# Kernel optimization log

Measured on AMD Instinct MI355X. Metric: run time of the kernel, lower is better.

The kernel has to match this reference:

```python
import math
import jax, jax.numpy as jnp
import numpy as np

TAU = 2.0
THR = 1.0
ALPHA = 10.0

T, B, IN_DIM, OUT_DIM = 64, 128, 2048, 2048


def setup_inputs() -> dict:
    key = jax.random.key(0)
    k1, k2, k3 = jax.random.split(key, 3)
    x_seq = jax.random.normal(k1, (T, B, IN_DIM), dtype=jnp.float32)
    # scale like nn.Linear default init so membrane potentials are O(1)
    W = jax.random.normal(k2, (OUT_DIM, IN_DIM), dtype=jnp.float32) / math.sqrt(IN_DIM)
    b = jax.random.normal(k3, (OUT_DIM,), dtype=jnp.float32) * 0.01
    return {"x_seq": x_seq, "W": W, "b": b}


def spike(x):
    # forward: hard threshold (surrogate gradient only matters in bwd)
    return (x > 0).astype(x.dtype)


def reference(x_seq, W, b):
    decay = math.exp(-1.0 / TAU)
    # hoist the linear layer out of the recurrence: one big GEMM
    cur_seq = jnp.einsum("tbi,oi->tbo", x_seq, W) + b  # (T, B, OUT_DIM)
    mem0 = jnp.zeros((x_seq.shape[1], W.shape[0]), dtype=x_seq.dtype)

    def step(mem, cur):
        mem = mem * decay + cur
        spk = spike(mem - THR)
        mem = mem - spk * THR
        return mem, spk

    _, spk_seq = jax.lax.scan(step, mem0, cur_seq)
    return spk_seq  # (T, B, OUT_DIM)
```

## Files before the change

### kernel.cpp

```cpp
#include <hip/hip_runtime.h>
#include <hip/hip_bf16.h>
#include <math.h>


typedef unsigned short u16;
typedef __attribute__((ext_vector_type(8))) short bf16x8;
typedef __attribute__((ext_vector_type(4))) float f32x4;

constexpr int T_STEPS = 64;
constexpr int BATCH   = 128;
constexpr int K_DIM   = 2048;
constexpr int N_DIM   = 2048;
constexpr int M_DIM   = T_STEPS * BATCH;
constexpr int NCHAIN  = BATCH * N_DIM;

constexpr float DECAY_F32 = (float)0.6065306597126334;
constexpr float BAND      = 2e-4f;

__global__ __launch_bounds__(512, 2)
void gemm_lif(const float* __restrict__ X, const float* __restrict__ W,
              const float* __restrict__ bias, float* __restrict__ out,
              unsigned int* __restrict__ counters,
              unsigned int* __restrict__ worklist) {
    extern __shared__ __align__(16) u16 smem[];
    u16* const sAh = smem;
    u16* const sAl = smem + 2 * 8192;
    u16* const sBh = smem + 4 * 8192;
    u16* const sBl = smem + 4 * 8192 + 2 * 4096;

    const int tid  = threadIdx.x;
    const int orig = blockIdx.x + gridDim.x * blockIdx.y;
    const int wg   = (orig & 7) * 64 + (orig >> 3);
    const int b0i  = (wg >> 4) * 4;
    const int n0   = (wg & 15) * 128;
    const int lane = tid & 63;
    const int wave = tid >> 6;
    const int wm   = wave >> 1;
    const int wn   = wave & 1;

    const int re   = (tid >> 6) * 16 + (tid & 15);
    const int ks_e = ((tid >> 4) & 3) * 8;
    const size_t a0f = (size_t)((re >> 2) * 128 + b0i + (re & 3)) * K_DIM + ks_e;
    const size_t a1f = (size_t)(((re >> 2) + 32) * 128 + b0i + (re & 3)) * K_DIM + ks_e;
    const size_t b0f = (size_t)(n0 + re) * K_DIM + ks_e;
    const int wA0 = tid * 8;
    const int wA1 = 4096 + tid * 8;
    const int wB0 = tid * 8;

    f32x4 acc[4][4];
#pragma unroll
    for (int i = 0; i < 4; i++)
#pragma unroll
        for (int j = 0; j < 4; j++) acc[i][j] = (f32x4){0.f, 0.f, 0.f, 0.f};

    float4 g0[6], g1[6];

#define GLOAD(SET, kc) do {                                                  \
        const size_t k_ = (size_t)(kc) * 32;                                 \
        g##SET[0] = *(const float4*)(X + a0f + k_);                          \
        g##SET[1] = *(const float4*)(X + a0f + k_ + 4);                      \
        g##SET[2] = *(const float4*)(X + a1f + k_);                          \
        g##SET[3] = *(const float4*)(X + a1f + k_ + 4);                      \
        g##SET[4] = *(const float4*)(W + b0f + k_);                          \
        g##SET[5] = *(const float4*)(W + b0f + k_ + 4);                      \
    } while (0)

#define DEK8(v0, v1, HI, LO) do {                                            \
        const float f_[8] = {v0.x, v0.y, v0.z, v0.w, v1.x, v1.y, v1.z, v1.w};\
        unsigned int hp_[4], lp_[4];                                         \
        _Pragma("unroll")                                                    \
        for (int q_ = 0; q_ < 8; q_ += 2) {                                  \
            u16 hh_[2], ll_[2];                                              \
            _Pragma("unroll")                                                \
            for (int e_ = 0; e_ < 2; e_++) {                                 \
                __hip_bfloat16 hb_ = __float2bfloat16(f_[q_ + e_]);          \
                const float hf_ = __bfloat162float(hb_);                     \
                __hip_bfloat16 lb_ = __float2bfloat16(f_[q_ + e_] - hf_);    \
                hh_[e_] = *(u16*)&hb_;                                       \
                ll_[e_] = *(u16*)&lb_;                                       \
            }                                                                \
            hp_[q_ >> 1] = (unsigned int)hh_[0] | ((unsigned int)hh_[1] << 16); \
            lp_[q_ >> 1] = (unsigned int)ll_[0] | ((unsigned int)ll_[1] << 16); \
        }                                                                    \
        HI = make_uint4(hp_[0], hp_[1], hp_[2], hp_[3]);                     \
        LO = make_uint4(lp_[0], lp_[1], lp_[2], lp_[3]);                     \
    } while (0)

#define CONVWRITE(s, SET) do {                                               \
        uint4 hA0_, lA0_, hA1_, lA1_, hB_, lB_;                              \
        DEK8(g##SET[0], g##SET[1], hA0_, lA0_);                              \
        DEK8(g##SET[2], g##SET[3], hA1_, lA1_);                              \
        DEK8(g##SET[4], g##SET[5], hB_, lB_);                                \
        *(uint4*)&sAh[(s) * 8192 + wA0] = hA0_;                              \
        *(uint4*)&sAl[(s) * 8192 + wA0] = lA0_;                              \
        *(uint4*)&sAh[(s) * 8192 + wA1] = hA1_;                              \
        *(uint4*)&sAl[(s) * 8192 + wA1] = lA1_;                              \
        *(uint4*)&sBh[(s) * 4096 + wB0] = hB_;                               \
        *(uint4*)&sBl[(s) * 4096 + wB0] = lB_;                               \
    } while (0)

#define COMPUTE(rs) do {                                                     \
        bf16x8 fah[4], fal[4], fbh[4], fbl[4];                               \
        _Pragma("unroll")                                                    \
        for (int ti = 0; ti < 4; ti++) {                                     \
            const int ta = wm * 4 + ti;                                      \
            fah[ti] = *(const bf16x8*)&sAh[(rs) * 8192 + (ta * 64 + lane) * 8]; \
            fal[ti] = *(const bf16x8*)&sAl[(rs) * 8192 + (ta * 64 + lane) * 8]; \
        }                                                                    \
        _Pragma("unroll")                                                    \
        for (int tj = 0; tj < 4; tj++) {                                     \
            const int tb = wn * 4 + tj;                                      \
            fbh[tj] = *(const bf16x8*)&sBh[(rs) * 4096 + (tb * 64 + lane) * 8]; \
            fbl[tj] = *(const bf16x8*)&sBl[(rs) * 4096 + (tb * 64 + lane) * 8]; \
        }                                                                    \
        __builtin_amdgcn_s_setprio(1);                                       \
        _Pragma("unroll")                                                    \
        for (int ti = 0; ti < 4; ti++)                                       \
        _Pragma("unroll")                                                    \
        for (int tj = 0; tj < 4; tj++) {                                     \
            acc[ti][tj] = __builtin_amdgcn_mfma_f32_16x16x32_bf16(           \
                fah[ti], fbh[tj], acc[ti][tj], 0, 0, 0);                     \
            acc[ti][tj] = __builtin_amdgcn_mfma_f32_16x16x32_bf16(           \
                fah[ti], fbl[tj], acc[ti][tj], 0, 0, 0);                     \
            acc[ti][tj] = __builtin_amdgcn_mfma_f32_16x16x32_bf16(           \
                fal[ti], fbh[tj], acc[ti][tj], 0, 0, 0);                     \
        }                                                                    \
        __builtin_amdgcn_s_setprio(0);                                       \
    } while (0)

#define BAR do {                                                             \
        __builtin_amdgcn_sched_barrier(0);                                   \
        __builtin_amdgcn_s_barrier();                                        \
        __builtin_amdgcn_sched_barrier(0);                                   \
    } while (0)
#define VMW(n) do {                                                          \
        asm volatile("s_waitcnt vmcnt(" #n ")" ::: "memory");                \
        __builtin_amdgcn_sched_barrier(0);                                   \
    } while (0)
#define LGKM0 do {                                                           \
        asm volatile("s_waitcnt lgkmcnt(0)" ::: "memory");                   \
        __builtin_amdgcn_sched_barrier(0);                                   \
    } while (0)

    GLOAD(0, 0);
    VMW(0);
    CONVWRITE(0, 0);
    GLOAD(1, 1);
    LGKM0;

    for (int kc = 0; kc < 60; kc += 2) {
        BAR;
        GLOAD(0, kc + 2);
        VMW(6);
        CONVWRITE(1, 1);
        LGKM0;
        COMPUTE(0);
        BAR;
        GLOAD(1, kc + 3);
        VMW(6);
        CONVWRITE(0, 0);
        LGKM0;
        COMPUTE(1);
    }
    BAR;
    GLOAD(0, 62);
    VMW(6);
    CONVWRITE(1, 1);
    LGKM0;
    COMPUTE(0);
    BAR;
    GLOAD(1, 63);
    VMW(6);
    CONVWRITE(0, 0);
    LGKM0;
    COMPUTE(1);
    BAR;
    VMW(0);
    CONVWRITE(1, 1);
    LGKM0;
    COMPUTE(0);
    BAR;
    COMPUTE(1);

#undef LGKM0
#undef VMW
#undef BAR
#undef COMPUTE
#undef CONVWRITE
#undef DEK8
#undef GLOAD

    __syncthreads();
    float* const curL = (float*)smem;

#pragma unroll
    for (int tj = 0; tj < 4; tj++) {
        const int col = wn * 64 + tj * 16 + (lane & 15);
        const float bv = bias[n0 + col];
#pragma unroll
        for (int ti = 0; ti < 4; ti++) {
            const int rb = wm * 64 + ti * 16 + (lane >> 4) * 4;
#pragma unroll
            for (int r = 0; r < 4; r++)
                curL[(rb + r) * 129 + col] = acc[ti][tj][r] + bv;
        }
    }
    __syncthreads();

    {
        const int bl  = tid >> 7;
        const int col = tid & 127;
        const int b   = b0i + bl;
        const int o   = n0 + col;
        float mem = 0.0f;
        bool flag = false;
#pragma unroll
        for (int t = 0; t < T_STEPS; t++) {
            const float cv = curL[(t * 4 + bl) * 129 + col];
            mem = __fadd_rn(__fmul_rn(mem, DECAY_F32), cv);
            const float d = __fsub_rn(mem, 1.0f);
            const bool spk = d > 0.0f;
            if (fabsf(d) < BAND) flag = true;
            out[(size_t)t * NCHAIN + (size_t)b * N_DIM + o] = spk ? 1.0f : 0.0f;
            if (spk) mem = __fsub_rn(mem, 1.0f);
        }
        if (flag) {
            const unsigned int p = atomicAdd(&counters[b], 1u);
            worklist[b * 2048 + p] = (unsigned int)o;
        }
    }
}

#define RG 16
#define RJ 4
#define BKR 64

__global__ __launch_bounds__(256)
void lif_repair2(const float* __restrict__ X, const float* __restrict__ W,
                 const float* __restrict__ bias,
                 const unsigned int* __restrict__ counters,
                 const unsigned int* __restrict__ worklist,
                 float* __restrict__ out) {
    __shared__ float sX[BKR][T_STEPS + 1];
    __shared__ float sW[RG][BKR + 1];
    __shared__ float scur[T_STEPS][RG + 1];
    __shared__ float sspk[T_STEPS][RG + 1];
    __shared__ int   so[RG];

    const int b = blockIdx.x / RJ;
    const int j = blockIdx.x % RJ;
    const unsigned int n_b = counters[b];
    if (n_b == 0) return;
    const int ngroups = (int)(n_b + RG - 1) / RG;

    const int tid = threadIdx.x;
    const int t   = tid & 63;
    const int oi  = tid >> 6;

    const int ts  = tid >> 2;
    const int kq  = (tid & 3) * 16;
    const int wo  = tid >> 4;
    const int wkq = (tid & 15) * 4;

    for (int g = j; g < ngroups; g += RJ) {
        if (tid < RG) {
            const int slot = g * RG + tid;
            so[tid] = (slot < (int)n_b) ? (int)worklist[b * 2048 + slot] : -1;
        }
        __syncthreads();

        float Csum[4] = {0.f, 0.f, 0.f, 0.f};
        float P[4]    = {0.f, 0.f, 0.f, 0.f};

        float4 rx[4];
        float4 rw;
        {
            const float* srcx = &X[(size_t)(ts * BATCH + b) * K_DIM + kq];
#pragma unroll
            for (int q = 0; q < 4; q++) rx[q] = *(const float4*)(srcx + q * 4);
            const int o = so[wo];
            rw = (o >= 0) ? *(const float4*)&W[(size_t)o * K_DIM + wkq]
                          : make_float4(0.f, 0.f, 0.f, 0.f);
        }

        for (int c = 0; c < K_DIM / BKR; c++) {
            if (c > 0 && (c % 5) == 0) {
#pragma unroll
                for (int q = 0; q < 4; q++) {
                    Csum[q] = __fadd_rn(Csum[q], P[q]);
                    P[q] = 0.f;
                }
            }
            __syncthreads();
#pragma unroll
            for (int q = 0; q < 4; q++) {
                sX[kq + q * 4 + 0][ts] = rx[q].x;
                sX[kq + q * 4 + 1][ts] = rx[q].y;
                sX[kq + q * 4 + 2][ts] = rx[q].z;
                sX[kq + q * 4 + 3][ts] = rx[q].w;
            }
            sW[wo][wkq + 0] = rw.x; sW[wo][wkq + 1] = rw.y;
            sW[wo][wkq + 2] = rw.z; sW[wo][wkq + 3] = rw.w;
            if (c + 1 < K_DIM / BKR) {
                const int k1 = (c + 1) * BKR;
                const float* srcx = &X[(size_t)(ts * BATCH + b) * K_DIM + k1 + kq];
#pragma unroll
                for (int q = 0; q < 4; q++) rx[q] = *(const float4*)(srcx + q * 4);
                const int o = so[wo];
                rw = (o >= 0) ? *(const float4*)&W[(size_t)o * K_DIM + k1 + wkq]
                              : make_float4(0.f, 0.f, 0.f, 0.f);
            }
            __syncthreads();
#pragma unroll 8
            for (int k = 0; k < BKR; k++) {
                const float xv = sX[k][t];
#pragma unroll
                for (int q = 0; q < 4; q++)
                    P[q] = fmaf(xv, sW[oi * 4 + q][k], P[q]);
            }
        }
        __syncthreads();
#pragma unroll
        for (int q = 0; q < 4; q++) {
            Csum[q] = __fadd_rn(Csum[q], P[q]);
            const int o = so[oi * 4 + q];
            scur[t][oi * 4 + q] = (o >= 0) ? __fadd_rn(Csum[q], bias[o]) : 0.f;
        }
        __syncthreads();
        if (tid < RG && so[tid] >= 0) {
            float mem = 0.0f;
            for (int tt = 0; tt < T_STEPS; tt++) {
                mem = __fadd_rn(__fmul_rn(mem, DECAY_F32), scur[tt][tid]);
                const float d = __fsub_rn(mem, 1.0f);
                const bool spk = d > 0.0f;
                sspk[tt][tid] = spk ? 1.0f : 0.0f;
                if (spk) mem = __fsub_rn(mem, 1.0f);
            }
        }
        __syncthreads();
#pragma unroll
        for (int q = 0; q < 4; q++) {
            const int o = so[oi * 4 + q];
            if (o >= 0)
                out[(size_t)t * NCHAIN + (size_t)b * N_DIM + o] = sspk[t][oi * 4 + q];
        }
        __syncthreads();
    }
}

__global__ __launch_bounds__(256)
void lif_openblas_q320(const float* __restrict__ X, const float* __restrict__ W,
                       const float* __restrict__ bias, float* __restrict__ out) {
    __shared__ float As[16][T_STEPS + 4];
    __shared__ float Ws[16][64 + 4];
    __shared__ float curbuf[T_STEPS][64 + 1];
    const int tid = threadIdx.x;
    const int o0 = blockIdx.x * 64, b0 = blockIdx.y;
    const int tm = (tid & 15) * 4, tn = (tid >> 4) * 4;
    float Csum[4][4], Pacc[4][4];
#pragma unroll
    for (int i = 0; i < 4; i++)
#pragma unroll
        for (int j = 0; j < 4; j++) { Csum[i][j] = 0.f; Pacc[i][j] = 0.f; }
    for (int c = 0; c < K_DIM / 16; c++) {
        if (c > 0 && (c % 20) == 0) {
#pragma unroll
            for (int i = 0; i < 4; i++)
#pragma unroll
                for (int j = 0; j < 4; j++) {
                    Csum[i][j] = __fadd_rn(Csum[i][j], Pacc[i][j]);
                    Pacc[i][j] = 0.f;
                }
        }
        const int k0 = c * 16;
        {
            const int t = tid >> 2, kq = (tid & 3) * 4;
            const float4 av = *(const float4*)&X[(size_t)(t * BATCH + b0) * K_DIM + k0 + kq];
            As[kq + 0][t] = av.x; As[kq + 1][t] = av.y;
            As[kq + 2][t] = av.z; As[kq + 3][t] = av.w;
            const float4 wv = *(const float4*)&W[(size_t)(o0 + t) * K_DIM + k0 + kq];
            Ws[kq + 0][t] = wv.x; Ws[kq + 1][t] = wv.y;
            Ws[kq + 2][t] = wv.z; Ws[kq + 3][t] = wv.w;
        }
        __syncthreads();
#pragma unroll
        for (int k = 0; k < 16; k++) {
            float a[4], w[4];
#pragma unroll
            for (int i = 0; i < 4; i++) a[i] = As[k][tm + i];
#pragma unroll
            for (int j = 0; j < 4; j++) w[j] = Ws[k][tn + j];
#pragma unroll
            for (int i = 0; i < 4; i++)
#pragma unroll
                for (int j = 0; j < 4; j++) Pacc[i][j] = fmaf(a[i], w[j], Pacc[i][j]);
        }
        __syncthreads();
    }
#pragma unroll
    for (int i = 0; i < 4; i++)
#pragma unroll
        for (int j = 0; j < 4; j++)
            curbuf[tm + i][tn + j] =
                __fadd_rn(__fadd_rn(Csum[i][j], Pacc[i][j]), bias[o0 + tn + j]);
    __syncthreads();
    if (tid < 64) {
        float mem = 0.0f;
#pragma unroll
        for (int t = 0; t < T_STEPS; t++) {
            mem = __fadd_rn(__fmul_rn(mem, DECAY_F32), curbuf[t][tid]);
            const float d = __fsub_rn(mem, 1.0f);
            const bool spk = d > 0.0f;
            out[(size_t)t * NCHAIN + (size_t)b0 * N_DIM + o0 + tid] = spk ? 1.0f : 0.0f;
            if (spk) mem = __fsub_rn(mem, 1.0f);
        }
    }
}

extern "C" void kernel_launch(void* const* d_in, const int* in_sizes, int n_in,
                              void* d_out, int out_size, void* d_ws, size_t ws_size,
                              hipStream_t stream) {
    const float* x = nullptr; const float* W = nullptr; const float* bias = nullptr;
    for (int i = 0; i < n_in; i++) {
        if      (in_sizes[i] == M_DIM * K_DIM) x    = (const float*)d_in[i];
        else if (in_sizes[i] == N_DIM * K_DIM) W    = (const float*)d_in[i];
        else if (in_sizes[i] == N_DIM)         bias = (const float*)d_in[i];
    }
    if (!x)    x    = (const float*)d_in[0];
    if (!W)    W    = (const float*)d_in[1];
    if (!bias) bias = (const float*)d_in[2];
    float* out = (float*)d_out;

    const size_t off_cnt = 0;
    const size_t off_wl  = 512;
    const size_t need    = off_wl + (size_t)128 * 2048 * 4;

    if (ws_size < need) {
        dim3 grid(N_DIM / 64, BATCH);
        lif_openblas_q320<<<grid, 256, 0, stream>>>(x, W, bias, out);
        return;
    }

    char* ws = (char*)d_ws;
    unsigned int* counters = (unsigned int*)(ws + off_cnt);
    unsigned int* worklist = (unsigned int*)(ws + off_wl);

    hipMemsetAsync(counters, 0, 512, stream);

    dim3 ggrid(N_DIM / 128, M_DIM / 256);
    gemm_lif<<<ggrid, 512, 132096, stream>>>(x, W, bias, out, counters, worklist);
    lif_repair2<<<128 * RJ, 256, 0, stream>>>(x, W, bias, counters, worklist, out);
}
```

Before: 417.7 us.

## Pre-split W into bf16 hi/lo planes and stream B tiles via global_load_lds

A new prologue kernel converts W once per call into separate bf16 high and low planes in workspace, and also zeroes the counters, which replaces the memset. The GEMM kernel then loads B tiles directly into LDS with global_load_lds and a three-deep B buffer. A tiles are still converted in registers. This removes the repeated per-block fp32-to-bf16 split of W and the register staging for B, at the cost of an extra kernel launch and extra workspace traffic.

```diff
diff --git a/kernel.cpp b/kernel.cpp
--- a/kernel.cpp
+++ b/kernel.cpp
@@ -17,8 +17,40 @@
 constexpr float DECAY_F32 = (float)0.6065306597126334;
 constexpr float BAND      = 2e-4f;
 
+#define GLDS16(g, l) __builtin_amdgcn_global_load_lds(                       \
+    (const __attribute__((address_space(1))) void*)(g),                      \
+    (__attribute__((address_space(3))) void*)(l), 16, 0, 0)
+
+__global__ __launch_bounds__(256)
+void wsplit(const float* __restrict__ W, u16* __restrict__ Wh,
+            u16* __restrict__ Wl, unsigned int* __restrict__ counters) {
+    if (blockIdx.x == 0 && threadIdx.x < 128) counters[threadIdx.x] = 0u;
+    const int base = blockIdx.x * 256 + threadIdx.x;
+    const float4 v0 = *(const float4*)(W + (size_t)base * 8);
+    const float4 v1 = *(const float4*)(W + (size_t)base * 8 + 4);
+    const float f[8] = {v0.x, v0.y, v0.z, v0.w, v1.x, v1.y, v1.z, v1.w};
+    unsigned int hp[4], lp[4];
+#pragma unroll
+    for (int q = 0; q < 8; q += 2) {
+        u16 hh[2], ll[2];
+#pragma unroll
+        for (int e = 0; e < 2; e++) {
+            __hip_bfloat16 hb = __float2bfloat16(f[q + e]);
+            const float hf = __bfloat162float(hb);
+            __hip_bfloat16 lb = __float2bfloat16(f[q + e] - hf);
+            hh[e] = *(u16*)&hb;
+            ll[e] = *(u16*)&lb;
+        }
+        hp[q >> 1] = (unsigned int)hh[0] | ((unsigned int)hh[1] << 16);
+        lp[q >> 1] = (unsigned int)ll[0] | ((unsigned int)ll[1] << 16);
+    }
+    *(uint4*)(Wh + (size_t)base * 8) = make_uint4(hp[0], hp[1], hp[2], hp[3]);
+    *(uint4*)(Wl + (size_t)base * 8) = make_uint4(lp[0], lp[1], lp[2], lp[3]);
+}
+
 __global__ __launch_bounds__(512, 2)
-void gemm_lif(const float* __restrict__ X, const float* __restrict__ W,
+void gemm_lif(const float* __restrict__ X,
+              const u16* __restrict__ Bh, const u16* __restrict__ Bl,
               const float* __restrict__ bias, float* __restrict__ out,
               unsigned int* __restrict__ counters,
               unsigned int* __restrict__ worklist) {
@@ -26,7 +58,7 @@
     u16* const sAh = smem;
     u16* const sAl = smem + 2 * 8192;
     u16* const sBh = smem + 4 * 8192;
-    u16* const sBl = smem + 4 * 8192 + 2 * 4096;
+    u16* const sBl = smem + 4 * 8192 + 3 * 4096;
 
     const int tid  = threadIdx.x;
     const int orig = blockIdx.x + gridDim.x * blockIdx.y;
@@ -45,7 +77,7 @@
     const size_t b0f = (size_t)(n0 + re) * K_DIM + ks_e;
     const int wA0 = tid * 8;
     const int wA1 = 4096 + tid * 8;
-    const int wB0 = tid * 8;
+    const int lB0 = wave * 512;
 
     f32x4 acc[4][4];
 #pragma unroll
@@ -53,16 +85,20 @@
 #pragma unroll
         for (int j = 0; j < 4; j++) acc[i][j] = (f32x4){0.f, 0.f, 0.f, 0.f};
 
-    float4 g0[6], g1[6];
-
-#define GLOAD(SET, kc) do {                                                  \
+    float4 g0[4], g1[4];
+
+#define GLOADA(SET, kc) do {                                                 \
         const size_t k_ = (size_t)(kc) * 32;                                 \
         g##SET[0] = *(const float4*)(X + a0f + k_);                          \
         g##SET[1] = *(const float4*)(X + a0f + k_ + 4);                      \
         g##SET[2] = *(const float4*)(X + a1f + k_);                          \
         g##SET[3] = *(const float4*)(X + a1f + k_ + 4);                      \
-        g##SET[4] = *(const float4*)(W + b0f + k_);                          \
-        g##SET[5] = *(const float4*)(W + b0f + k_ + 4);                      \
+    } while (0)
+
+#define GLDSB(bs, kc) do {                                                   \
+        const size_t k_ = (size_t)(kc) * 32;                                 \
+        GLDS16(Bh + b0f + k_, sBh + (bs) * 4096 + lB0);                      \
+        GLDS16(Bl + b0f + k_, sBl + (bs) * 4096 + lB0);                      \
     } while (0)
 
 #define DEK8(v0, v1, HI, LO) do {                                            \
@@ -86,32 +122,29 @@
         LO = make_uint4(lp_[0], lp_[1], lp_[2], lp_[3]);                     \
     } while (0)
 
-#define CONVWRITE(s, SET) do {                                               \
-        uint4 hA0_, lA0_, hA1_, lA1_, hB_, lB_;                              \
+#define CONVWA(s, SET) do {                                                  \
+        uint4 hA0_, lA0_, hA1_, lA1_;                                        \
         DEK8(g##SET[0], g##SET[1], hA0_, lA0_);                              \
         DEK8(g##SET[2], g##SET[3], hA1_, lA1_);                              \
-        DEK8(g##SET[4], g##SET[5], hB_, lB_);                                \
         *(uint4*)&sAh[(s) * 8192 + wA0] = hA0_;                              \
         *(uint4*)&sAl[(s) * 8192 + wA0] = lA0_;                              \
         *(uint4*)&sAh[(s) * 8192 + wA1] = hA1_;                              \
         *(uint4*)&sAl[(s) * 8192 + wA1] = lA1_;                              \
-        *(uint4*)&sBh[(s) * 4096 + wB0] = hB_;                               \
-        *(uint4*)&sBl[(s) * 4096 + wB0] = lB_;                               \
-    } while (0)
-
-#define COMPUTE(rs) do {                                                     \
+    } while (0)
+
+#define COMPUTE(ra, rb) do {                                                 \
         bf16x8 fah[4], fal[4], fbh[4], fbl[4];                               \
         _Pragma("unroll")                                                    \
         for (int ti = 0; ti < 4; ti++) {                                     \
             const int ta = wm * 4 + ti;                                      \
-            fah[ti] = *(const bf16x8*)&sAh[(rs) * 8192 + (ta * 64 + lane) * 8]; \
-            fal[ti] = *(const bf16x8*)&sAl[(rs) * 8192 + (ta * 64 + lane) * 8]; \
+            fah[ti] = *(const bf16x8*)&sAh[(ra) * 8192 + (ta * 64 + lane) * 8]; \
+            fal[ti] = *(const bf16x8*)&sAl[(ra) * 8192 + (ta * 64 + lane) * 8]; \
         }                                                                    \
         _Pragma("unroll")                                                    \
         for (int tj = 0; tj < 4; tj++) {                                     \
             const int tb = wn * 4 + tj;                                      \
-            fbh[tj] = *(const bf16x8*)&sBh[(rs) * 4096 + (tb * 64 + lane) * 8]; \
-            fbl[tj] = *(const bf16x8*)&sBl[(rs) * 4096 + (tb * 64 + lane) * 8]; \
+            fbh[tj] = *(const bf16x8*)&sBh[(rb) * 4096 + (tb * 64 + lane) * 8]; \
+            fbl[tj] = *(const bf16x8*)&sBl[(rb) * 4096 + (tb * 64 + lane) * 8]; \
         }                                                                    \
         __builtin_amdgcn_s_setprio(1);                                       \
         _Pragma("unroll")                                                    \
@@ -142,53 +175,44 @@
         __builtin_amdgcn_sched_barrier(0);                                   \
     } while (0)
 
-    GLOAD(0, 0);
-    VMW(0);
-    CONVWRITE(0, 0);
-    GLOAD(1, 1);
+    GLOADA(0, 0);
+    GLDSB(0, 0);
+    GLOADA(1, 1);
+    GLDSB(1, 1);
+    VMW(6);
+    CONVWA(0, 0);
     LGKM0;
 
-    for (int kc = 0; kc < 60; kc += 2) {
-        BAR;
-        GLOAD(0, kc + 2);
-        VMW(6);
-        CONVWRITE(1, 1);
-        LGKM0;
-        COMPUTE(0);
-        BAR;
-        GLOAD(1, kc + 3);
-        VMW(6);
-        CONVWRITE(0, 0);
-        LGKM0;
-        COMPUTE(1);
-    }
-    BAR;
-    GLOAD(0, 62);
-    VMW(6);
-    CONVWRITE(1, 1);
-    LGKM0;
-    COMPUTE(0);
-    BAR;
-    GLOAD(1, 63);
-    VMW(6);
-    CONVWRITE(0, 0);
-    LGKM0;
-    COMPUTE(1);
-    BAR;
-    VMW(0);
-    CONVWRITE(1, 1);
-    LGKM0;
-    COMPUTE(0);
-    BAR;
-    COMPUTE(1);
+    for (int kcb = 0; kcb < 60; kcb += 6) {
+        BAR;  GLOADA(0, kcb + 2);  GLDSB(2, kcb + 2);  VMW(6);
+        CONVWA(1, 1);  LGKM0;  COMPUTE(0, 0);
+        BAR;  GLOADA(1, kcb + 3);  GLDSB(0, kcb + 3);  VMW(6);
+        CONVWA(0, 0);  LGKM0;  COMPUTE(1, 1);
+        BAR;  GLOADA(0, kcb + 4);  GLDSB(1, kcb + 4);  VMW(6);
+        CONVWA(1, 1);  LGKM0;  COMPUTE(0, 2);
+        BAR;  GLOADA(1, kcb + 5);  GLDSB(2, kcb + 5);  VMW(6);
+        CONVWA(0, 0);  LGKM0;  COMPUTE(1, 0);
+        BAR;  GLOADA(0, kcb + 6);  GLDSB(0, kcb + 6);  VMW(6);
+        CONVWA(1, 1);  LGKM0;  COMPUTE(0, 1);
+        BAR;  GLOADA(1, kcb + 7);  GLDSB(1, kcb + 7);  VMW(6);
+        CONVWA(0, 0);  LGKM0;  COMPUTE(1, 2);
+    }
+    BAR;  GLOADA(0, 62);  GLDSB(2, 62);  VMW(6);
+    CONVWA(1, 1);  LGKM0;  COMPUTE(0, 0);
+    BAR;  GLOADA(1, 63);  GLDSB(0, 63);  VMW(6);
+    CONVWA(0, 0);  LGKM0;  COMPUTE(1, 1);
+    BAR;  VMW(0);
+    CONVWA(1, 1);  LGKM0;  COMPUTE(0, 2);
+    BAR;  COMPUTE(1, 0);
 
 #undef LGKM0
 #undef VMW
 #undef BAR
 #undef COMPUTE
-#undef CONVWRITE
+#undef CONVWA
 #undef DEK8
-#undef GLOAD
+#undef GLDSB
+#undef GLOADA
 
     __syncthreads();
     float* const curL = (float*)smem;
@@ -433,7 +457,10 @@
 
     const size_t off_cnt = 0;
     const size_t off_wl  = 512;
-    const size_t need    = off_wl + (size_t)128 * 2048 * 4;
+    const size_t off_Wh  = off_wl + (size_t)128 * 2048 * 4;
+    const size_t szW     = (size_t)N_DIM * K_DIM * 2;
+    const size_t off_Wl  = off_Wh + szW;
+    const size_t need    = off_Wl + szW;
 
     if (ws_size < need) {
         dim3 grid(N_DIM / 64, BATCH);
@@ -444,10 +471,11 @@
     char* ws = (char*)d_ws;
     unsigned int* counters = (unsigned int*)(ws + off_cnt);
     unsigned int* worklist = (unsigned int*)(ws + off_wl);
-
-    hipMemsetAsync(counters, 0, 512, stream);
-
+    u16* Wh = (u16*)(ws + off_Wh);
+    u16* Wl = (u16*)(ws + off_Wl);
+
+    wsplit<<<(N_DIM * K_DIM / 8) / 256, 256, 0, stream>>>(W, Wh, Wl, counters);
     dim3 ggrid(N_DIM / 128, M_DIM / 256);
-    gemm_lif<<<ggrid, 512, 132096, stream>>>(x, W, bias, out, counters, worklist);
+    gemm_lif<<<ggrid, 512, 132096, stream>>>(x, Wh, Wl, bias, out, counters, worklist);
     lif_repair2<<<128 * RJ, 256, 0, stream>>>(x, W, bias, counters, worklist, out);
 }
```

Result: slower. 577.1 us (+38.2%).
